# Kernel optimization log

Measured on AMD Instinct MI355X. Metric: run time of the kernel, lower is better.

## Reference

```python
import jax, jax.numpy as jnp
import numpy as np

WS = 8          # window_size
SHIFT = 4       # shift_size
HEADS = 12
C = 384
HD = C // HEADS
SCALE = HD ** -0.5
N = WS * WS


def _rel_pos_index(Wh, Ww):
    # double_step_seq(2*Ww-1, Wh, 1, Ww) -> (1, Wh*Ww); idx = rel + rel.T; flip along axis 1
    seq1 = np.arange(0, (2 * Ww - 1) * Wh, 2 * Ww - 1)
    seq2 = np.arange(0, Ww)
    rel = (seq1[:, None] + seq2[None, :]).reshape(1, -1)
    idx = rel + rel.T
    return np.flip(idx, 1).copy()

REL_IDX = jnp.asarray(_rel_pos_index(WS, WS))  # [N, N] int


def window_partition(x, ws):
    # x: [B, H, W, C] -> [B*nW, ws*ws, C]
    B, H, W, Cc = x.shape
    x = x.reshape(B, H // ws, ws, W // ws, ws, Cc).transpose(0, 1, 3, 2, 4, 5)
    return x.reshape(-1, ws * ws, Cc)


def window_reverse(win, H, W, ws):
    B = win.shape[0] // ((H // ws) * (W // ws))
    x = win.reshape(B, H // ws, W // ws, ws, ws, -1).transpose(0, 1, 3, 2, 4, 5)
    return x.reshape(B, H, W, -1)


def _attn_mask(H, W, ws, shift):
    # region ids 0..8 per (h,w) as in the torch slice loop
    hi = np.arange(H)
    wi = np.arange(W)
    h_id = (hi >= H - ws).astype(np.int32) + (hi >= H - shift).astype(np.int32)
    w_id = (wi >= W - ws).astype(np.int32) + (wi >= W - shift).astype(np.int32)
    cnt = (h_id[:, None] * 3 + w_id[None, :]).astype(np.float32)
    img = jnp.asarray(cnt)[None, :, :, None]              # [1, H, W, 1]
    mw = window_partition(img, ws).reshape(-1, ws * ws)   # [nW, N]
    diff = mw[:, None, :] - mw[:, :, None]                # [nW, N, N]
    return jnp.where(diff != 0, jnp.float32(-100.0), jnp.float32(0.0))


def setup_inputs() -> dict:
    key = jax.random.key(0)
    ks = jax.random.split(key, 8)
    B, H, W = 16, 96, 96
    std = 0.02
    return {
        "query": jax.random.normal(ks[0], (B, H * W, C), jnp.float32),
        "skip_query": jax.random.normal(ks[1], (B, H * W, C), jnp.float32),
        "W_qkv": jax.random.normal(ks[2], (C, 2 * C), jnp.float32) * std,
        "b_qkv": jnp.zeros((2 * C,), jnp.float32),
        "W_skip": jax.random.normal(ks[3], (C, C), jnp.float32) * std,
        "b_skip": jnp.zeros((C,), jnp.float32),
        "rpb_table": jax.random.normal(ks[4], ((2 * WS - 1) * (2 * WS - 1), HEADS), jnp.float32) * std,
        "W_proj": jax.random.normal(ks[5], (C, C), jnp.float32) * std,
        "b_proj": jnp.zeros((C,), jnp.float32),
        "h": H,
        "w": W,
    }


def reference(query, skip_query, W_qkv, b_qkv, W_skip, b_skip, rpb_table, W_proj, b_proj, h, w):
    B, L, Cc = query.shape
    q4 = query.reshape(B, h, w, Cc)
    s4 = skip_query.reshape(B, h, w, Cc)
    pad_r = (WS - w % WS) % WS
    pad_b = (WS - h % WS) % WS
    q4 = jnp.pad(q4, ((0, 0), (0, pad_b), (0, pad_r), (0, 0)))
    s4 = jnp.pad(s4, ((0, 0), (0, pad_b), (0, pad_r), (0, 0)))
    H_pad, W_pad = q4.shape[1], q4.shape[2]

    # cyclic shift
    q4 = jnp.roll(q4, (-SHIFT, -SHIFT), axis=(1, 2))
    s4 = jnp.roll(s4, (-SHIFT, -SHIFT), axis=(1, 2))
    mask = _attn_mask(H_pad, W_pad, WS, SHIFT)  # [nW, N, N]

    xw = window_partition(q4, WS)   # [Bn, N, C] -> k, v source
    sw = window_partition(s4, WS)   # [Bn, N, C] -> q source
    Bn = xw.shape[0]

    kv = (xw @ W_qkv + b_qkv).reshape(Bn, N, 2, HEADS, HD)
    k = kv[:, :, 0].transpose(0, 2, 1, 3)   # [Bn, H, N, d]
    v = kv[:, :, 1].transpose(0, 2, 1, 3)
    q = ((sw @ W_skip + b_skip).reshape(Bn, N, HEADS, HD).transpose(0, 2, 1, 3)) * SCALE

    attn = jnp.einsum('bhnd,bhmd->bhnm', q, k)  # [Bn, H, N, N]
    rpb = rpb_table[REL_IDX.reshape(-1)].reshape(N, N, HEADS).transpose(2, 0, 1)
    attn = attn + rpb[None]
    nW = mask.shape[0]
    attn = (attn.reshape(B, nW, HEADS, N, N) + mask[None, :, None]).reshape(Bn, HEADS, N, N)
    attn = jax.nn.softmax(attn, axis=-1)

    out = jnp.einsum('bhnm,bhmd->bhnd', attn, v).transpose(0, 2, 1, 3).reshape(Bn, N, Cc)
    out = out @ W_proj + b_proj

    x4 = window_reverse(out.reshape(-1, WS, WS, Cc), H_pad, W_pad, WS)
    x4 = jnp.roll(x4, (SHIFT, SHIFT), axis=(1, 2))
    x4 = x4[:, :h, :w]
    return x4.reshape(B, h * w, Cc)
```

## Files before the change

### kernel.cpp

```cpp
#include <hip/hip_runtime.h>
#include <hip/hip_bf16.h>


typedef __attribute__((ext_vector_type(8))) short short8;
typedef __attribute__((ext_vector_type(4))) float floatx4;

#define MFMA16(a, b, c) __builtin_amdgcn_mfma_f32_16x16x32_bf16(a, b, c, 0, 0, 0)

__device__ __forceinline__ short f2bf(float f) {
    __hip_bfloat16 h = __float2bfloat16(f);
    return *reinterpret_cast<short*>(&h);
}

__device__ __forceinline__ unsigned cvt2bf(float lo, float hi) {
    unsigned r;
    asm("v_cvt_pk_bf16_f32 %0, %1, %2" : "=v"(r) : "v"(lo), "v"(hi));
    return r;
}

__device__ __forceinline__ void glds16(const void* g, void* l) {
    __builtin_amdgcn_global_load_lds(
        (const __attribute__((address_space(1))) void*)g,
        (__attribute__((address_space(3))) void*)l, 16, 0, 0);
}

__device__ __forceinline__ void lds_fence() {
    asm volatile("s_waitcnt lgkmcnt(0)" ::: "memory");
    __builtin_amdgcn_sched_barrier(0);
}


__global__ __launch_bounds__(256) void prep_wt(const float* __restrict__ Wqkv,
                                               const float* __restrict__ Wskip,
                                               short* __restrict__ Wt) {
    int tid = blockIdx.x * 256 + threadIdx.x;
    if (tid >= 384 * 144) return;
    int k = tid / 144;
    int n8 = (tid % 144) * 8;
#pragma unroll
    for (int e = 0; e < 8; e++) {
        int n = n8 + e;
        float v = (n < 768) ? Wqkv[k * 768 + n]
                            : Wskip[k * 384 + (n - 768)] * 0.17677669529663687f;
        Wt[(size_t)n * 384 + k] = f2bf(v);
    }
}

__global__ __launch_bounds__(256) void prep_wtp(const float* __restrict__ Wproj,
                                                short* __restrict__ WtP) {
    int tid = blockIdx.x * 256 + threadIdx.x;
    if (tid >= 384 * 48) return;
    int k = tid / 48;
    int n8 = (tid % 48) * 8;
#pragma unroll
    for (int e = 0; e < 8; e++) {
        int n = n8 + e;
        WtP[(size_t)n * 384 + k] = f2bf(Wproj[k * 384 + n]);
    }
}

__global__ __launch_bounds__(256) void prep_bias(const float* __restrict__ rpb,
                                                 float* __restrict__ bias64) {
    int tid = blockIdx.x * 256 + threadIdx.x;
    if (tid >= 49152) return;
    int h = tid >> 12;
    int rem = tid & 4095;
    int i = rem >> 6, kk = rem & 63;
    int j = 63 - kk;
    int ridx = 15 * (i >> 3) + (i & 7) + 15 * (j >> 3) + (j & 7);
    bias64[tid] = rpb[ridx * 12 + h];
}

__global__ __launch_bounds__(768, 1) void fused_win(
    const float* __restrict__ xq, const float* __restrict__ xs,
    const short* __restrict__ Wt, const short* __restrict__ WtP,
    const float* __restrict__ bqkv, const float* __restrict__ bskip,
    const float* __restrict__ bproj, const float* __restrict__ bias64,
    float* __restrict__ out) {
    __shared__ short smem[73728];

    const int win = blockIdx.x;
    const int tid = threadIdx.x, lane = tid & 63, wid = tid >> 6;
    const int l15 = lane & 15, g4 = lane >> 4;
    const int al7 = l15 & 7;
    const int brd = (g4 ^ ((l15 ^ (l15 >> 2)) & 3)) * 8;

    const int b_img = win / 144, wr = win % 144;
    const int wy = wr / 12, wx = wr % 12;

    const int gr = tid / 12, gj = tid - gr * 12;
    int gyy = wy * 8 + (gr >> 3) + 4; if (gyy >= 96) gyy -= 96;
    int gxx = wx * 8 + (gr & 7) + 4;  if (gxx >= 96) gxx -= 96;
    const size_t grow = ((size_t)b_img * 9216 + gyy * 96 + gxx) * 384;
    short* lrow = smem + gr * 384;
    const int gr7 = gr & 7;

    auto gatherA = [&](const float* src) {
        const float* rb = src + grow;
#pragma unroll
        for (int cc = 0; cc < 4; cc++) {
            int c = gj * 4 + cc;
            float4 f0 = *(const float4*)(rb + c * 8);
            float4 f1 = *(const float4*)(rb + c * 8 + 4);
            uint4 u;
            u.x = cvt2bf(f0.x, f0.y); u.y = cvt2bf(f0.z, f0.w);
            u.z = cvt2bf(f1.x, f1.y); u.w = cvt2bf(f1.z, f1.w);
            *(uint4*)(lrow + ((c ^ gr7) * 8)) = u;
        }
    };

    const int swst = ((lane >> 2) ^ (lane >> 4)) & 3;
    int bso[2];
#pragma unroll
    for (int j = 0; j < 2; j++)
        bso[j] = (j * 16 + (lane >> 2)) * 384 + (((lane & 3) ^ swst) * 8);
    short* wsc = smem + 24576 + wid * 4096;

    const short* sK = Wt + (size_t)(wid * 32) * 384;
    const short* sV = Wt + (size_t)(384 + wid * 32) * 384;
    const short* sQ = Wt + (size_t)(768 + wid * 32) * 384;
    const short* sP = WtP + (size_t)(wid * 32) * 384;

#pragma unroll
    for (int s = 0; s < 2; s++)
#pragma unroll
        for (int j = 0; j < 2; j++)
            glds16(sQ + bso[j] + s * 32, wsc + s * 1024 + j * 512);
    gatherA(xs);
    float4 xr[8];
    {
        const float* rb = xq + grow;
#pragma unroll
        for (int cc = 0; cc < 4; cc++) {
            xr[cc * 2]     = *(const float4*)(rb + (gj * 4 + cc) * 8);
            xr[cc * 2 + 1] = *(const float4*)(rb + (gj * 4 + cc) * 8 + 4);
        }
    }
    __syncthreads();

    floatx4 aq[2][4];
#pragma unroll
    for (int a = 0; a < 2; a++)
#pragma unroll
        for (int b = 0; b < 4; b++)
#pragma unroll
            for (int r = 0; r < 4; r++) aq[a][b][r] = 0.f;
#pragma unroll
    for (int kt = 0; kt < 12; ++kt) {
        if (kt == 11) asm volatile("s_waitcnt vmcnt(0)" ::: "memory");
        else          asm volatile("s_waitcnt vmcnt(2)" ::: "memory");
        const int choff = ((kt * 4 + g4) ^ al7) * 8;
        short* hb = wsc + (kt & 1) * 1024;
        short8 af[4], bq[2];
#pragma unroll
        for (int b = 0; b < 4; b++)
            af[b] = *(const short8*)(smem + (b * 16 + l15) * 384 + choff);
#pragma unroll
        for (int a = 0; a < 2; a++)
            bq[a] = *(const short8*)(hb + (a * 16 + l15) * 32 + brd);
        __builtin_amdgcn_sched_barrier(0);
        asm volatile("s_waitcnt lgkmcnt(0)" ::: "memory");
        if (kt < 10) {
            int ko = (kt + 2) * 32;
#pragma unroll
            for (int j = 0; j < 2; j++) glds16(sQ + bso[j] + ko, hb + j * 512);
        }
        __builtin_amdgcn_sched_barrier(0);
#pragma unroll
        for (int a = 0; a < 2; a++)
#pragma unroll
            for (int b = 0; b < 4; b++)
                aq[a][b] = MFMA16(bq[a], af[b], aq[a][b]);
    }

    const float scl = 0.17677669529663687f;
#pragma unroll
    for (int a = 0; a < 2; a++) {
        float4 bv = *(const float4*)(bskip + wid * 32 + a * 16 + g4 * 4);
#pragma unroll
        for (int b = 0; b < 4; b++) {
            uint2 pk;
            pk.x = cvt2bf(aq[a][b][0] + bv.x * scl, aq[a][b][1] + bv.y * scl);
            pk.y = cvt2bf(aq[a][b][2] + bv.z * scl, aq[a][b][3] + bv.w * scl);
            int row = b * 16 + l15;
            int phys = (a * 2 + (g4 >> 1)) ^ (row & 3);
            *(uint2*)(wsc + 1024 + row * 32 + phys * 8 + (g4 & 1) * 4) = pk;
        }
    }
    short8 qf[4];
#pragma unroll
    for (int nj = 0; nj < 4; nj++) {
        int row = nj * 16 + l15;
        qf[nj] = *(const short8*)(wsc + 1024 + row * 32 + ((g4 ^ (row & 3)) * 8));
    }
    lds_fence();

#pragma unroll
    for (int s = 0; s < 2; s++)
#pragma unroll
        for (int j = 0; j < 2; j++) {
            glds16(sK + bso[j] + s * 32, wsc + s * 2048 + j * 512);
            glds16(sV + bso[j] + s * 32, wsc + s * 2048 + 1024 + j * 512);
        }
    __syncthreads();
#pragma unroll
    for (int cc = 0; cc < 4; cc++) {
        int c = gj * 4 + cc;
        uint4 u;
        u.x = cvt2bf(xr[cc * 2].x, xr[cc * 2].y);
        u.y = cvt2bf(xr[cc * 2].z, xr[cc * 2].w);
        u.z = cvt2bf(xr[cc * 2 + 1].x, xr[cc * 2 + 1].y);
        u.w = cvt2bf(xr[cc * 2 + 1].z, xr[cc * 2 + 1].w);
        *(uint4*)(lrow + ((c ^ gr7) * 8)) = u;
    }
    __syncthreads();

    floatx4 ak[2][4], av[2][4];
#pragma unroll
    for (int a = 0; a < 2; a++)
#pragma unroll
        for (int b = 0; b < 4; b++)
#pragma unroll
            for (int r = 0; r < 4; r++) { ak[a][b][r] = 0.f; av[a][b][r] = 0.f; }
#pragma unroll
    for (int kt = 0; kt < 12; ++kt) {
        if (kt == 11) asm volatile("s_waitcnt vmcnt(0)" ::: "memory");
        else          asm volatile("s_waitcnt vmcnt(4)" ::: "memory");
        const int choff = ((kt * 4 + g4) ^ al7) * 8;
        short* hb = wsc + (kt & 1) * 2048;
        short8 af[4], bk[2], bv2[2];
#pragma unroll
        for (int b = 0; b < 4; b++)
            af[b] = *(const short8*)(smem + (b * 16 + l15) * 384 + choff);
#pragma unroll
        for (int a = 0; a < 2; a++) {
            bk[a]  = *(const short8*)(hb + (a * 16 + l15) * 32 + brd);
            bv2[a] = *(const short8*)(hb + 1024 + (a * 16 + l15) * 32 + brd);
        }
        __builtin_amdgcn_sched_barrier(0);
        asm volatile("s_waitcnt lgkmcnt(0)" ::: "memory");
        if (kt < 10) {
            int ko = (kt + 2) * 32;
#pragma unroll
            for (int j = 0; j < 2; j++) {
                glds16(sK + bso[j] + ko, hb + j * 512);
                glds16(sV + bso[j] + ko, hb + 1024 + j * 512);
            }
        }
        __builtin_amdgcn_sched_barrier(0);
#pragma unroll
        for (int a = 0; a < 2; a++)
#pragma unroll
            for (int b = 0; b < 4; b++) {
                ak[a][b] = MFMA16(bk[a], af[b], ak[a][b]);
                av[a][b] = MFMA16(af[b], bv2[a], av[a][b]);
            }
    }
    __syncthreads();

#pragma unroll
    for (int a = 0; a < 2; a++) {
        float4 bv = *(const float4*)(bqkv + wid * 32 + a * 16 + g4 * 4);
#pragma unroll
        for (int b = 0; b < 4; b++) {
            uint2 pk;
            pk.x = cvt2bf(ak[a][b][0] + bv.x, ak[a][b][1] + bv.y);
            pk.y = cvt2bf(ak[a][b][2] + bv.z, ak[a][b][3] + bv.w);
            int row = b * 16 + l15;
            int phys = (a * 2 + (g4 >> 1)) ^ (row & 3);
            *(uint2*)(wsc + row * 32 + phys * 8 + (g4 & 1) * 4) = pk;
        }
    }
#pragma unroll
    for (int a = 0; a < 2; a++) {
        float bvs = bqkv[384 + wid * 32 + a * 16 + l15];
#pragma unroll
        for (int b = 0; b < 4; b++) {
            uint2 pk;
            pk.x = cvt2bf(av[a][b][0] + bvs, av[a][b][1] + bvs);
            pk.y = cvt2bf(av[a][b][2] + bvs, av[a][b][3] + bvs);
            int tch = b * 2 + (g4 >> 1);
            *(uint2*)(wsc + 2048 + (a * 16 + l15) * 64 +
                      ((tch ^ (l15 & 7)) * 8) + (g4 & 1) * 4) = pk;
        }
    }
    short8 kf[4], vf[2][2];
#pragma unroll
    for (int mi = 0; mi < 4; mi++) {
        int row = mi * 16 + l15;
        kf[mi] = *(const short8*)(wsc + row * 32 + ((g4 ^ (row & 3)) * 8));
    }
#pragma unroll
    for (int ma = 0; ma < 2; ma++)
#pragma unroll
        for (int ks = 0; ks < 2; ks++)
            vf[ma][ks] = *(const short8*)(wsc + 2048 + (ma * 16 + l15) * 64 +
                                          (((ks * 4 + g4) ^ (l15 & 7)) * 8));

    floatx4 st[4][4];
#pragma unroll
    for (int mi = 0; mi < 4; mi++)
#pragma unroll
        for (int nj = 0; nj < 4; nj++)
#pragma unroll
            for (int r = 0; r < 4; r++) st[mi][nj][r] = 0.f;
#pragma unroll
    for (int mi = 0; mi < 4; mi++)
#pragma unroll
        for (int nj = 0; nj < 4; nj++)
            st[mi][nj] = MFMA16(kf[mi], qf[nj], st[mi][nj]);

    const float* bb = bias64 + wid * 4096;
#pragma unroll
    for (int nj = 0; nj < 4; nj++) {
        int i = nj * 16 + l15;
#pragma unroll
        for (int mi = 0; mi < 4; mi++) {
            floatx4 b4 = *(const floatx4*)(bb + i * 64 + mi * 16 + g4 * 4);
            st[mi][nj] += b4;
        }
    }

    if (wy == 11 || wx == 11) {
        int wy11 = (wy == 11), wx11 = (wx == 11);
        int ri[4];
#pragma unroll
        for (int nj = 0; nj < 4; nj++) {
            int t = nj * 16 + l15;
            int hh = wy11 ? (((t >> 3) >= 4) ? 2 : 1) : 0;
            int ww = wx11 ? (((t & 7) >= 4) ? 2 : 1) : 0;
            ri[nj] = hh * 3 + ww;
        }
#pragma unroll
        for (int mi = 0; mi < 4; mi++)
#pragma unroll
            for (int r = 0; r < 4; r++) {
                int t = mi * 16 + g4 * 4 + r;
                int hh = wy11 ? (((t >> 3) >= 4) ? 2 : 1) : 0;
                int ww = wx11 ? (((t & 7) >= 4) ? 2 : 1) : 0;
                int rk = hh * 3 + ww;
#pragma unroll
                for (int nj = 0; nj < 4; nj++)
                    if (rk != ri[nj]) st[mi][nj][r] -= 100.0f;
            }
    }

    float rden[4];
#pragma unroll
    for (int nj = 0; nj < 4; nj++) {
        float m = -1e30f;
#pragma unroll
        for (int mi = 0; mi < 4; mi++)
#pragma unroll
            for (int r = 0; r < 4; r++) m = fmaxf(m, st[mi][nj][r]);
        m = fmaxf(m, __shfl_xor(m, 16));
        m = fmaxf(m, __shfl_xor(m, 32));
        float s = 0.f;
#pragma unroll
        for (int mi = 0; mi < 4; mi++)
#pragma unroll
            for (int r = 0; r < 4; r++) {
                float p = __expf(st[mi][nj][r] - m);
                st[mi][nj][r] = p;
                s += p;
            }
        s += __shfl_xor(s, 16);
        s += __shfl_xor(s, 32);
        rden[nj] = 1.0f / s;
    }

#pragma unroll
    for (int mi = 0; mi < 4; mi++)
#pragma unroll
        for (int nj = 0; nj < 4; nj++) {
            uint2 pk;
            pk.x = cvt2bf(st[mi][nj][0], st[mi][nj][1]);
            pk.y = cvt2bf(st[mi][nj][2], st[mi][nj][3]);
            int kch = mi * 2 + (g4 >> 1);
            *(uint2*)(wsc + (nj * 16 + l15) * 64 +
                      ((kch ^ (l15 & 7)) * 8) + (g4 & 1) * 4) = pk;
        }

    floatx4 o[2][4];
#pragma unroll
    for (int ma = 0; ma < 2; ma++)
#pragma unroll
        for (int nj = 0; nj < 4; nj++)
#pragma unroll
            for (int r = 0; r < 4; r++) o[ma][nj][r] = 0.f;
#pragma unroll
    for (int ks = 0; ks < 2; ks++) {
        short8 pb[4];
#pragma unroll
        for (int nj = 0; nj < 4; nj++)
            pb[nj] = *(const short8*)(wsc + (nj * 16 + l15) * 64 +
                                      (((ks * 4 + g4) ^ (l15 & 7)) * 8));
#pragma unroll
        for (int ma = 0; ma < 2; ma++)
#pragma unroll
            for (int nj = 0; nj < 4; nj++)
                o[ma][nj] = MFMA16(vf[ma][ks], pb[nj], o[ma][nj]);
    }
    lds_fence();

#pragma unroll
    for (int s = 0; s < 2; s++)
#pragma unroll
        for (int j = 0; j < 2; j++)
            glds16(sP + bso[j] + s * 32, wsc + s * 1024 + j * 512);

#pragma unroll
    for (int ma = 0; ma < 2; ma++)
#pragma unroll
        for (int nj = 0; nj < 4; nj++) {
            int i = nj * 16 + l15;
            uint2 pk;
            pk.x = cvt2bf(o[ma][nj][0] * rden[nj], o[ma][nj][1] * rden[nj]);
            pk.y = cvt2bf(o[ma][nj][2] * rden[nj], o[ma][nj][3] * rden[nj]);
            int ch = wid * 4 + ma * 2 + (g4 >> 1);
            *(uint2*)(smem + i * 384 + ((ch ^ (i & 7)) * 8) + (g4 & 1) * 4) = pk;
        }
    __syncthreads();

    floatx4 ap[2][4];
#pragma unroll
    for (int a = 0; a < 2; a++)
#pragma unroll
        for (int b = 0; b < 4; b++)
#pragma unroll
            for (int r = 0; r < 4; r++) ap[a][b][r] = 0.f;
#pragma unroll
    for (int kt = 0; kt < 12; ++kt) {
        if (kt == 11) asm volatile("s_waitcnt vmcnt(0)" ::: "memory");
        else          asm volatile("s_waitcnt vmcnt(2)" ::: "memory");
        const int choff = ((kt * 4 + g4) ^ al7) * 8;
        short* hb = wsc + (kt & 1) * 1024;
        short8 af[4], bp[2];
#pragma unroll
        for (int b = 0; b < 4; b++)
            af[b] = *(const short8*)(smem + (b * 16 + l15) * 384 + choff);
#pragma unroll
        for (int a = 0; a < 2; a++)
            bp[a] = *(const short8*)(hb + (a * 16 + l15) * 32 + brd);
        __builtin_amdgcn_sched_barrier(0);
        asm volatile("s_waitcnt lgkmcnt(0)" ::: "memory");
        if (kt < 10) {
            int ko = (kt + 2) * 32;
#pragma unroll
            for (int j = 0; j < 2; j++) glds16(sP + bso[j] + ko, hb + j * 512);
        }
        __builtin_amdgcn_sched_barrier(0);
#pragma unroll
        for (int a = 0; a < 2; a++)
#pragma unroll
            for (int b = 0; b < 4; b++)
                ap[a][b] = MFMA16(bp[a], af[b], ap[a][b]);
    }

    float* fsc = (float*)wsc;
#pragma unroll
    for (int a = 0; a < 2; a++) {
        float4 bv = *(const float4*)(bproj + wid * 32 + a * 16 + g4 * 4);
#pragma unroll
        for (int b = 0; b < 4; b++) {
            int row = b * 16 + l15;
            int phys = (a * 4 + g4) ^ (row & 7);
            floatx4 ov = ap[a][b];
            ov[0] += bv.x; ov[1] += bv.y; ov[2] += bv.z; ov[3] += bv.w;
            *(floatx4*)(fsc + row * 32 + phys * 4) = ov;
        }
    }
    lds_fence();
    {
        const int r8 = lane >> 3, c8 = lane & 7;
#pragma unroll
        for (int it = 0; it < 8; it++) {
            int row = it * 8 + r8;
            floatx4 ov = *(const floatx4*)(fsc + row * 32 + ((c8 ^ r8) * 4));
            int yy = wy * 8 + (row >> 3) + 4; if (yy >= 96) yy -= 96;
            int xx = wx * 8 + (row & 7) + 4;  if (xx >= 96) xx -= 96;
            *(floatx4*)(&out[((size_t)b_img * 9216 + yy * 96 + xx) * 384 +
                             wid * 32 + c8 * 4]) = ov;
        }
    }
}

extern "C" void kernel_launch(void* const* d_in, const int* in_sizes, int n_in,
                              void* d_out, int out_size, void* d_ws, size_t ws_size,
                              hipStream_t stream) {
    const float* query = (const float*)d_in[0];
    const float* skipq = (const float*)d_in[1];
    const float* Wqkv  = (const float*)d_in[2];
    const float* bqkv  = (const float*)d_in[3];
    const float* Wskip = (const float*)d_in[4];
    const float* bskip = (const float*)d_in[5];
    const float* rpb   = (const float*)d_in[6];
    const float* Wproj = (const float*)d_in[7];
    const float* bproj = (const float*)d_in[8];
    float* out = (float*)d_out;

    int M = in_sizes[0] / 384;
    int nwin = M / 64;

    char* ws = (char*)d_ws;
    size_t off = 0;
    auto alloc = [&](size_t bytes) -> void* {
        void* p = ws + off;
        off = (off + bytes + 255) & ~(size_t)255;
        return p;
    };
    short* Wt     = (short*)alloc((size_t)1152 * 384 * 2);
    short* WtP    = (short*)alloc((size_t)384 * 384 * 2);
    float* bias64 = (float*)alloc((size_t)12 * 64 * 64 * 4);
    (void)ws_size;

    hipLaunchKernelGGL(prep_wt, dim3(216), dim3(256), 0, stream, Wqkv, Wskip, Wt);
    hipLaunchKernelGGL(prep_wtp, dim3(72), dim3(256), 0, stream, Wproj, WtP);
    hipLaunchKernelGGL(prep_bias, dim3(192), dim3(256), 0, stream, rpb, bias64);
    hipLaunchKernelGGL(fused_win, dim3(nwin), dim3(768), 0, stream,
                       query, skipq, Wt, WtP, bqkv, bskip, bproj, bias64, out);
}
```

Measured before the change: 464.7 us.

## Halve LDS footprint to fit two workgroups per CU

Shrinks shared memory by single-buffering weight tiles, splitting the fused K/V projection into separate K and V passes, and staging Q/K/P/output transposes through smaller per-wave scratch in halves. Launch bounds are raised to request higher occupancy. The aim is to let multiple 768-thread blocks co-reside per CU to hide latency. In exchange it loses the double-buffered prefetch overlap, re-reads A fragments for separate K and V loops, adds fences and barriers, and risks register spills from the tighter register budget.

```diff
diff --git a/kernel.cpp b/kernel.cpp
--- a/kernel.cpp
+++ b/kernel.cpp
@@ -71,13 +71,13 @@
     bias64[tid] = rpb[ridx * 12 + h];
 }
 
-__global__ __launch_bounds__(768, 1) void fused_win(
+__global__ __launch_bounds__(768, 6) void fused_win(
     const float* __restrict__ xq, const float* __restrict__ xs,
     const short* __restrict__ Wt, const short* __restrict__ WtP,
     const float* __restrict__ bqkv, const float* __restrict__ bskip,
     const float* __restrict__ bproj, const float* __restrict__ bias64,
     float* __restrict__ out) {
-    __shared__ short smem[73728];
+    __shared__ short smem[36864];
 
     const int win = blockIdx.x;
     const int tid = threadIdx.x, lane = tid & 63, wid = tid >> 6;
@@ -95,8 +95,23 @@
     short* lrow = smem + gr * 384;
     const int gr7 = gr & 7;
 
-    auto gatherA = [&](const float* src) {
-        const float* rb = src + grow;
+    const int swst = ((lane >> 2) ^ (lane >> 4)) & 3;
+    int bso[2];
+#pragma unroll
+    for (int j = 0; j < 2; j++)
+        bso[j] = (j * 16 + (lane >> 2)) * 384 + (((lane & 3) ^ swst) * 8);
+    short* wsc = smem + 24576 + wid * 1024;
+    short* pA  = smem + wid * 2048;
+
+    const short* sK = Wt + (size_t)(wid * 32) * 384;
+    const short* sV = Wt + (size_t)(384 + wid * 32) * 384;
+    const short* sQ = Wt + (size_t)(768 + wid * 32) * 384;
+    const short* sP = WtP + (size_t)(wid * 32) * 384;
+
+#pragma unroll
+    for (int j = 0; j < 2; j++) glds16(sQ + bso[j], wsc + j * 512);
+    {
+        const float* rb = xs + grow;
 #pragma unroll
         for (int cc = 0; cc < 4; cc++) {
             int c = gj * 4 + cc;
@@ -107,26 +122,7 @@
             u.z = cvt2bf(f1.x, f1.y); u.w = cvt2bf(f1.z, f1.w);
             *(uint4*)(lrow + ((c ^ gr7) * 8)) = u;
         }
-    };
-
-    const int swst = ((lane >> 2) ^ (lane >> 4)) & 3;
-    int bso[2];
-#pragma unroll
-    for (int j = 0; j < 2; j++)
-        bso[j] = (j * 16 + (lane >> 2)) * 384 + (((lane & 3) ^ swst) * 8);
-    short* wsc = smem + 24576 + wid * 4096;
-
-    const short* sK = Wt + (size_t)(wid * 32) * 384;
-    const short* sV = Wt + (size_t)(384 + wid * 32) * 384;
-    const short* sQ = Wt + (size_t)(768 + wid * 32) * 384;
-    const short* sP = WtP + (size_t)(wid * 32) * 384;
-
-#pragma unroll
-    for (int s = 0; s < 2; s++)
-#pragma unroll
-        for (int j = 0; j < 2; j++)
-            glds16(sQ + bso[j] + s * 32, wsc + s * 1024 + j * 512);
-    gatherA(xs);
+    }
     float4 xr[8];
     {
         const float* rb = xq + grow;
@@ -147,23 +143,21 @@
             for (int r = 0; r < 4; r++) aq[a][b][r] = 0.f;
 #pragma unroll
     for (int kt = 0; kt < 12; ++kt) {
-        if (kt == 11) asm volatile("s_waitcnt vmcnt(0)" ::: "memory");
-        else          asm volatile("s_waitcnt vmcnt(2)" ::: "memory");
+        asm volatile("s_waitcnt vmcnt(0)" ::: "memory");
         const int choff = ((kt * 4 + g4) ^ al7) * 8;
-        short* hb = wsc + (kt & 1) * 1024;
         short8 af[4], bq[2];
 #pragma unroll
         for (int b = 0; b < 4; b++)
             af[b] = *(const short8*)(smem + (b * 16 + l15) * 384 + choff);
 #pragma unroll
         for (int a = 0; a < 2; a++)
-            bq[a] = *(const short8*)(hb + (a * 16 + l15) * 32 + brd);
+            bq[a] = *(const short8*)(wsc + (a * 16 + l15) * 32 + brd);
         __builtin_amdgcn_sched_barrier(0);
         asm volatile("s_waitcnt lgkmcnt(0)" ::: "memory");
-        if (kt < 10) {
-            int ko = (kt + 2) * 32;
-#pragma unroll
-            for (int j = 0; j < 2; j++) glds16(sQ + bso[j] + ko, hb + j * 512);
+        if (kt < 11) {
+            int ko = (kt + 1) * 32;
+#pragma unroll
+            for (int j = 0; j < 2; j++) glds16(sQ + bso[j] + ko, wsc + j * 512);
         }
         __builtin_amdgcn_sched_barrier(0);
 #pragma unroll
@@ -174,34 +168,33 @@
     }
 
     const float scl = 0.17677669529663687f;
-#pragma unroll
-    for (int a = 0; a < 2; a++) {
-        float4 bv = *(const float4*)(bskip + wid * 32 + a * 16 + g4 * 4);
-#pragma unroll
-        for (int b = 0; b < 4; b++) {
-            uint2 pk;
-            pk.x = cvt2bf(aq[a][b][0] + bv.x * scl, aq[a][b][1] + bv.y * scl);
-            pk.y = cvt2bf(aq[a][b][2] + bv.z * scl, aq[a][b][3] + bv.w * scl);
-            int row = b * 16 + l15;
-            int phys = (a * 2 + (g4 >> 1)) ^ (row & 3);
-            *(uint2*)(wsc + 1024 + row * 32 + phys * 8 + (g4 & 1) * 4) = pk;
-        }
-    }
     short8 qf[4];
 #pragma unroll
-    for (int nj = 0; nj < 4; nj++) {
-        int row = nj * 16 + l15;
-        qf[nj] = *(const short8*)(wsc + 1024 + row * 32 + ((g4 ^ (row & 3)) * 8));
-    }
-    lds_fence();
-
-#pragma unroll
-    for (int s = 0; s < 2; s++)
-#pragma unroll
-        for (int j = 0; j < 2; j++) {
-            glds16(sK + bso[j] + s * 32, wsc + s * 2048 + j * 512);
-            glds16(sV + bso[j] + s * 32, wsc + s * 2048 + 1024 + j * 512);
-        }
+    for (int jq = 0; jq < 2; jq++) {
+#pragma unroll
+        for (int a = 0; a < 2; a++) {
+            float4 bv = *(const float4*)(bskip + wid * 32 + a * 16 + g4 * 4);
+#pragma unroll
+            for (int bb = 0; bb < 2; bb++) {
+                int b = jq * 2 + bb;
+                uint2 pk;
+                pk.x = cvt2bf(aq[a][b][0] + bv.x * scl, aq[a][b][1] + bv.y * scl);
+                pk.y = cvt2bf(aq[a][b][2] + bv.z * scl, aq[a][b][3] + bv.w * scl);
+                int lr = bb * 16 + l15;
+                int phys = (a * 2 + (g4 >> 1)) ^ (l15 & 3);
+                *(uint2*)(wsc + lr * 32 + phys * 8 + (g4 & 1) * 4) = pk;
+            }
+        }
+        lds_fence();
+#pragma unroll
+        for (int nn = 0; nn < 2; nn++)
+            qf[jq * 2 + nn] = *(const short8*)(wsc + (nn * 16 + l15) * 32 +
+                                               ((g4 ^ (l15 & 3)) * 8));
+        lds_fence();
+    }
+
+#pragma unroll
+    for (int j = 0; j < 2; j++) glds16(sK + bso[j], wsc + j * 512);
     __syncthreads();
 #pragma unroll
     for (int cc = 0; cc < 4; cc++) {
@@ -215,62 +208,100 @@
     }
     __syncthreads();
 
-    floatx4 ak[2][4], av[2][4];
+    floatx4 ak[2][4];
 #pragma unroll
     for (int a = 0; a < 2; a++)
 #pragma unroll
         for (int b = 0; b < 4; b++)
 #pragma unroll
-            for (int r = 0; r < 4; r++) { ak[a][b][r] = 0.f; av[a][b][r] = 0.f; }
+            for (int r = 0; r < 4; r++) ak[a][b][r] = 0.f;
 #pragma unroll
     for (int kt = 0; kt < 12; ++kt) {
-        if (kt == 11) asm volatile("s_waitcnt vmcnt(0)" ::: "memory");
-        else          asm volatile("s_waitcnt vmcnt(4)" ::: "memory");
+        asm volatile("s_waitcnt vmcnt(0)" ::: "memory");
         const int choff = ((kt * 4 + g4) ^ al7) * 8;
-        short* hb = wsc + (kt & 1) * 2048;
-        short8 af[4], bk[2], bv2[2];
+        short8 af[4], bk[2];
 #pragma unroll
         for (int b = 0; b < 4; b++)
             af[b] = *(const short8*)(smem + (b * 16 + l15) * 384 + choff);
 #pragma unroll
+        for (int a = 0; a < 2; a++)
+            bk[a] = *(const short8*)(wsc + (a * 16 + l15) * 32 + brd);
+        __builtin_amdgcn_sched_barrier(0);
+        asm volatile("s_waitcnt lgkmcnt(0)" ::: "memory");
+        if (kt < 11) {
+            int ko = (kt + 1) * 32;
+#pragma unroll
+            for (int j = 0; j < 2; j++) glds16(sK + bso[j] + ko, wsc + j * 512);
+        }
+        __builtin_amdgcn_sched_barrier(0);
+#pragma unroll
+        for (int a = 0; a < 2; a++)
+#pragma unroll
+            for (int b = 0; b < 4; b++)
+                ak[a][b] = MFMA16(bk[a], af[b], ak[a][b]);
+    }
+
+    short8 kf[4];
+#pragma unroll
+    for (int jq = 0; jq < 2; jq++) {
+#pragma unroll
         for (int a = 0; a < 2; a++) {
-            bk[a]  = *(const short8*)(hb + (a * 16 + l15) * 32 + brd);
-            bv2[a] = *(const short8*)(hb + 1024 + (a * 16 + l15) * 32 + brd);
-        }
+            float4 bv = *(const float4*)(bqkv + wid * 32 + a * 16 + g4 * 4);
+#pragma unroll
+            for (int bb = 0; bb < 2; bb++) {
+                int b = jq * 2 + bb;
+                uint2 pk;
+                pk.x = cvt2bf(ak[a][b][0] + bv.x, ak[a][b][1] + bv.y);
+                pk.y = cvt2bf(ak[a][b][2] + bv.z, ak[a][b][3] + bv.w);
+                int lr = bb * 16 + l15;
+                int phys = (a * 2 + (g4 >> 1)) ^ (l15 & 3);
+                *(uint2*)(wsc + lr * 32 + phys * 8 + (g4 & 1) * 4) = pk;
+            }
+        }
+        lds_fence();
+#pragma unroll
+        for (int nn = 0; nn < 2; nn++)
+            kf[jq * 2 + nn] = *(const short8*)(wsc + (nn * 16 + l15) * 32 +
+                                               ((g4 ^ (l15 & 3)) * 8));
+        lds_fence();
+    }
+
+#pragma unroll
+    for (int j = 0; j < 2; j++) glds16(sV + bso[j], wsc + j * 512);
+    floatx4 av[2][4];
+#pragma unroll
+    for (int a = 0; a < 2; a++)
+#pragma unroll
+        for (int b = 0; b < 4; b++)
+#pragma unroll
+            for (int r = 0; r < 4; r++) av[a][b][r] = 0.f;
+#pragma unroll
+    for (int kt = 0; kt < 12; ++kt) {
+        asm volatile("s_waitcnt vmcnt(0)" ::: "memory");
+        const int choff = ((kt * 4 + g4) ^ al7) * 8;
+        short8 af[4], bv2[2];
+#pragma unroll
+        for (int b = 0; b < 4; b++)
+            af[b] = *(const short8*)(smem + (b * 16 + l15) * 384 + choff);
+#pragma unroll
+        for (int a = 0; a < 2; a++)
+            bv2[a] = *(const short8*)(wsc + (a * 16 + l15) * 32 + brd);
         __builtin_amdgcn_sched_barrier(0);
         asm volatile("s_waitcnt lgkmcnt(0)" ::: "memory");
-        if (kt < 10) {
-            int ko = (kt + 2) * 32;
-#pragma unroll
-            for (int j = 0; j < 2; j++) {
-                glds16(sK + bso[j] + ko, hb + j * 512);
-                glds16(sV + bso[j] + ko, hb + 1024 + j * 512);
-            }
-        }
-        __builtin_amdgcn_sched_barrier(0);
-#pragma unroll
-        for (int a = 0; a < 2; a++)
-#pragma unroll
-            for (int b = 0; b < 4; b++) {
-                ak[a][b] = MFMA16(bk[a], af[b], ak[a][b]);
+        if (kt < 11) {
+            int ko = (kt + 1) * 32;
+#pragma unroll
+            for (int j = 0; j < 2; j++) glds16(sV + bso[j] + ko, wsc + j * 512);
+        }
+        __builtin_amdgcn_sched_barrier(0);
+#pragma unroll
+        for (int a = 0; a < 2; a++)
+#pragma unroll
+            for (int b = 0; b < 4; b++)
                 av[a][b] = MFMA16(af[b], bv2[a], av[a][b]);
-            }
-    }
-    __syncthreads();
-
-#pragma unroll
-    for (int a = 0; a < 2; a++) {
-        float4 bv = *(const float4*)(bqkv + wid * 32 + a * 16 + g4 * 4);
-#pragma unroll
-        for (int b = 0; b < 4; b++) {
-            uint2 pk;
-            pk.x = cvt2bf(ak[a][b][0] + bv.x, ak[a][b][1] + bv.y);
-            pk.y = cvt2bf(ak[a][b][2] + bv.z, ak[a][b][3] + bv.w);
-            int row = b * 16 + l15;
-            int phys = (a * 2 + (g4 >> 1)) ^ (row & 3);
-            *(uint2*)(wsc + row * 32 + phys * 8 + (g4 & 1) * 4) = pk;
-        }
-    }
+    }
+    __syncthreads();
+
 #pragma unroll
     for (int a = 0; a < 2; a++) {
         float bvs = bqkv[384 + wid * 32 + a * 16 + l15];
@@ -280,22 +311,19 @@
             pk.x = cvt2bf(av[a][b][0] + bvs, av[a][b][1] + bvs);
             pk.y = cvt2bf(av[a][b][2] + bvs, av[a][b][3] + bvs);
             int tch = b * 2 + (g4 >> 1);
-            *(uint2*)(wsc + 2048 + (a * 16 + l15) * 64 +
+            *(uint2*)(pA + (a * 16 + l15) * 64 +
                       ((tch ^ (l15 & 7)) * 8) + (g4 & 1) * 4) = pk;
         }
     }
-    short8 kf[4], vf[2][2];
-#pragma unroll
-    for (int mi = 0; mi < 4; mi++) {
-        int row = mi * 16 + l15;
-        kf[mi] = *(const short8*)(wsc + row * 32 + ((g4 ^ (row & 3)) * 8));
-    }
+    lds_fence();
+    short8 vf[2][2];
 #pragma unroll
     for (int ma = 0; ma < 2; ma++)
 #pragma unroll
         for (int ks = 0; ks < 2; ks++)
-            vf[ma][ks] = *(const short8*)(wsc + 2048 + (ma * 16 + l15) * 64 +
+            vf[ma][ks] = *(const short8*)(pA + (ma * 16 + l15) * 64 +
                                           (((ks * 4 + g4) ^ (l15 & 7)) * 8));
+    lds_fence();
 
     floatx4 st[4][4];
 #pragma unroll
@@ -369,18 +397,6 @@
         rden[nj] = 1.0f / s;
     }
 
-#pragma unroll
-    for (int mi = 0; mi < 4; mi++)
-#pragma unroll
-        for (int nj = 0; nj < 4; nj++) {
-            uint2 pk;
-            pk.x = cvt2bf(st[mi][nj][0], st[mi][nj][1]);
-            pk.y = cvt2bf(st[mi][nj][2], st[mi][nj][3]);
-            int kch = mi * 2 + (g4 >> 1);
-            *(uint2*)(wsc + (nj * 16 + l15) * 64 +
-                      ((kch ^ (l15 & 7)) * 8) + (g4 & 1) * 4) = pk;
-        }
-
     floatx4 o[2][4];
 #pragma unroll
     for (int ma = 0; ma < 2; ma++)
@@ -390,24 +406,36 @@
             for (int r = 0; r < 4; r++) o[ma][nj][r] = 0.f;
 #pragma unroll
     for (int ks = 0; ks < 2; ks++) {
+#pragma unroll
+        for (int mm = 0; mm < 2; mm++) {
+            int mi = ks * 2 + mm;
+#pragma unroll
+            for (int nj = 0; nj < 4; nj++) {
+                uint2 pk;
+                pk.x = cvt2bf(st[mi][nj][0], st[mi][nj][1]);
+                pk.y = cvt2bf(st[mi][nj][2], st[mi][nj][3]);
+                int phys = (mm * 2 + (g4 >> 1)) ^ (l15 & 3);
+                *(uint2*)(pA + (nj * 16 + l15) * 32 + phys * 8 + (g4 & 1) * 4) = pk;
+            }
+        }
+        lds_fence();
         short8 pb[4];
 #pragma unroll
         for (int nj = 0; nj < 4; nj++)
-            pb[nj] = *(const short8*)(wsc + (nj * 16 + l15) * 64 +
-                                      (((ks * 4 + g4) ^ (l15 & 7)) * 8));
+            pb[nj] = *(const short8*)(pA + (nj * 16 + l15) * 32 +
+                                      ((g4 ^ (l15 & 3)) * 8));
 #pragma unroll
         for (int ma = 0; ma < 2; ma++)
 #pragma unroll
             for (int nj = 0; nj < 4; nj++)
                 o[ma][nj] = MFMA16(vf[ma][ks], pb[nj], o[ma][nj]);
-    }
-    lds_fence();
-
-#pragma unroll
-    for (int s = 0; s < 2; s++)
-#pragma unroll
-        for (int j = 0; j < 2; j++)
-            glds16(sP + bso[j] + s * 32, wsc + s * 1024 + j * 512);
+        lds_fence();
+    }
+
+#pragma unroll
+    for (int j = 0; j < 2; j++) glds16(sP + bso[j], wsc + j * 512);
+
+    __syncthreads();
 
 #pragma unroll
     for (int ma = 0; ma < 2; ma++)
@@ -431,23 +459,21 @@
             for (int r = 0; r < 4; r++) ap[a][b][r] = 0.f;
 #pragma unroll
     for (int kt = 0; kt < 12; ++kt) {
-        if (kt == 11) asm volatile("s_waitcnt vmcnt(0)" ::: "memory");
-        else          asm volatile("s_waitcnt vmcnt(2)" ::: "memory");
+        asm volatile("s_waitcnt vmcnt(0)" ::: "memory");
         const int choff = ((kt * 4 + g4) ^ al7) * 8;
-        short* hb = wsc + (kt & 1) * 1024;
         short8 af[4], bp[2];
 #pragma unroll
         for (int b = 0; b < 4; b++)
             af[b] = *(const short8*)(smem + (b * 16 + l15) * 384 + choff);
 #pragma unroll
         for (int a = 0; a < 2; a++)
-            bp[a] = *(const short8*)(hb + (a * 16 + l15) * 32 + brd);
+            bp[a] = *(const short8*)(wsc + (a * 16 + l15) * 32 + brd);
         __builtin_amdgcn_sched_barrier(0);
         asm volatile("s_waitcnt lgkmcnt(0)" ::: "memory");
-        if (kt < 10) {
-            int ko = (kt + 2) * 32;
-#pragma unroll
-            for (int j = 0; j < 2; j++) glds16(sP + bso[j] + ko, hb + j * 512);
+        if (kt < 11) {
+            int ko = (kt + 1) * 32;
+#pragma unroll
+            for (int j = 0; j < 2; j++) glds16(sP + bso[j] + ko, wsc + j * 512);
         }
         __builtin_amdgcn_sched_barrier(0);
 #pragma unroll
@@ -456,32 +482,39 @@
             for (int b = 0; b < 4; b++)
                 ap[a][b] = MFMA16(bp[a], af[b], ap[a][b]);
     }
-
-    float* fsc = (float*)wsc;
-#pragma unroll
-    for (int a = 0; a < 2; a++) {
-        float4 bv = *(const float4*)(bproj + wid * 32 + a * 16 + g4 * 4);
-#pragma unroll
-        for (int b = 0; b < 4; b++) {
-            int row = b * 16 + l15;
-            int phys = (a * 4 + g4) ^ (row & 7);
-            floatx4 ov = ap[a][b];
-            ov[0] += bv.x; ov[1] += bv.y; ov[2] += bv.z; ov[3] += bv.w;
-            *(floatx4*)(fsc + row * 32 + phys * 4) = ov;
-        }
-    }
-    lds_fence();
-    {
-        const int r8 = lane >> 3, c8 = lane & 7;
-#pragma unroll
-        for (int it = 0; it < 8; it++) {
-            int row = it * 8 + r8;
-            floatx4 ov = *(const floatx4*)(fsc + row * 32 + ((c8 ^ r8) * 4));
-            int yy = wy * 8 + (row >> 3) + 4; if (yy >= 96) yy -= 96;
-            int xx = wx * 8 + (row & 7) + 4;  if (xx >= 96) xx -= 96;
-            *(floatx4*)(&out[((size_t)b_img * 9216 + yy * 96 + xx) * 384 +
-                             wid * 32 + c8 * 4]) = ov;
-        }
+    __syncthreads();
+
+    float* fsc = (float*)pA;
+#pragma unroll
+    for (int h = 0; h < 2; h++) {
+#pragma unroll
+        for (int a = 0; a < 2; a++) {
+            float4 bv = *(const float4*)(bproj + wid * 32 + a * 16 + g4 * 4);
+#pragma unroll
+            for (int bb = 0; bb < 2; bb++) {
+                int b = h * 2 + bb;
+                int lr = bb * 16 + l15;
+                int phys = (a * 4 + g4) ^ (lr & 7);
+                floatx4 ov = ap[a][b];
+                ov[0] += bv.x; ov[1] += bv.y; ov[2] += bv.z; ov[3] += bv.w;
+                *(floatx4*)(fsc + lr * 32 + phys * 4) = ov;
+            }
+        }
+        lds_fence();
+        {
+            const int r8 = lane >> 3, c8 = lane & 7;
+#pragma unroll
+            for (int it = 0; it < 4; it++) {
+                int lr = it * 8 + r8;
+                floatx4 ov = *(const floatx4*)(fsc + lr * 32 + ((c8 ^ r8) * 4));
+                int trow = h * 32 + lr;
+                int yy = wy * 8 + (trow >> 3) + 4; if (yy >= 96) yy -= 96;
+                int xx = wx * 8 + (trow & 7) + 4;  if (xx >= 96) xx -= 96;
+                *(floatx4*)(&out[((size_t)b_img * 9216 + yy * 96 + xx) * 384 +
+                                 wid * 32 + c8 * 4]) = ov;
+            }
+        }
+        lds_fence();
     }
 }
 
```

After: 823.8 us. +77.3%, slower.
